# Performance work log

Measured on AMD Instinct MI355X. Metric: run time of the kernel, lower is better.

## Reference

```python
import jax, jax.numpy as jnp
import numpy as np

NUM_CLUSTERS = 10
NUM_ITERS = 10
EPS = 1e-6


def setup_inputs() -> dict:
    key = jax.random.key(0)
    k1, _ = jax.random.split(key)
    features = jax.random.normal(k1, (64, 500, 2048), dtype=jnp.float32)
    p = jnp.ones((1,), dtype=jnp.float32) * 3.0  # GeM learnable exponent
    return {"features": features, "p": p}


def reference(features, p):
    # features: [B, N, D]; k-means (10 iters) then per-cluster GeM pooling.
    B, N, D = features.shape
    K = NUM_CLUSTERS
    init_centroids = features[:, :K, :]
    f_sq = jnp.sum(features * features, axis=-1, keepdims=True)  # [B,N,1]

    def step(centroids, _):
        # squared euclidean distances [B,N,K] (argmin identical to cdist argmin)
        d2 = (f_sq
              - 2.0 * jnp.einsum('bnd,bkd->bnk', features, centroids)
              + jnp.sum(centroids * centroids, axis=-1)[:, None, :])
        assign = jnp.argmin(d2, axis=2)                      # [B,N]
        onehot = jax.nn.one_hot(assign, K, dtype=features.dtype)  # [B,N,K]
        counts = jnp.maximum(onehot.sum(axis=1), 1.0)        # [B,K]
        new_c = jnp.einsum('bnk,bnd->bkd', onehot, features) / counts[..., None]
        return new_c, assign

    centroids, assigns = jax.lax.scan(step, init_centroids, None, length=NUM_ITERS)
    # torch code uses assignments from the LAST iteration (pre-final-update centroids)
    assignments = assigns[-1]                                # [B,N]

    onehot = jax.nn.one_hot(assignments, K, dtype=features.dtype)  # [B,N,K]
    counts = onehot.sum(axis=1)                              # [B,K]
    # GeM within each cluster: mean over cluster points of clamp(x,eps)^p, then ^(1/p)
    powed = jnp.clip(features, EPS, None) ** p               # [B,N,D]
    mean_pow = jnp.einsum('bnk,bnd->bkd', onehot, powed) / jnp.maximum(counts, 1.0)[..., None]
    gem = mean_pow ** (1.0 / p)                              # [B,K,D]
    # empty clusters fall back to the centroid
    out = jnp.where((counts > 0)[..., None], gem, centroids)
    return out
```

## Files before the change

kernel.cpp:

```cpp
#include <hip/hip_runtime.h>

#define NB 64
#define NPTS 500
#define ND 2048
#define NK 10
#define NITERS 10
#define FEPS 1e-6f

__global__ __launch_bounds__(256) void init_kernel(const float* __restrict__ f,
                                                   float* __restrict__ cent,
                                                   int* __restrict__ counts)
{
    int gid = blockIdx.x * 256 + threadIdx.x;
    if (gid < NITERS * NB * NK) counts[gid] = 0;

    const int total4 = NB * NK * ND / 4;
    for (int i = gid; i < total4; i += gridDim.x * 256) {
        int d4 = i & (ND / 4 - 1);
        int bk = i >> 9;
        int b = bk / NK, k = bk - b * NK;
        ((float4*)cent)[i] =
            ((const float4*)(f + ((size_t)b * NPTS + k) * ND))[d4];
    }
}

__global__ __launch_bounds__(256) void assign_kernel(const float* __restrict__ f,
                                                     const float* __restrict__ cent,
                                                     int* __restrict__ assign,
                                                     int* __restrict__ counts_it)
{
    const int b    = blockIdx.y;
    const int wv   = threadIdx.x >> 6;
    const int lane = threadIdx.x & 63;
    const int n0   = blockIdx.x * 8 + wv * 2;
    const int n1   = n0 + 1;
    const bool v0  = (n0 < NPTS), v1 = (n1 < NPTS);

    const float4* f4 = (const float4*)(f + (size_t)b * NPTS * ND);
    const float4  z4 = make_float4(0.f, 0.f, 0.f, 0.f);
    float4 fa[8], fb[8];
#pragma unroll
    for (int j = 0; j < 8; ++j) {
        int idx = j * 64 + lane;
        fa[j] = v0 ? f4[(size_t)n0 * 512 + idx] : z4;
        fb[j] = v1 ? f4[(size_t)n1 * 512 + idx] : z4;
    }

    const float4* c4 = (const float4*)(cent + (size_t)b * NK * ND);
    float sA[NK], sB[NK];
#pragma unroll
    for (int k = 0; k < NK; ++k) {
        float a0 = 0.f, a1 = 0.f, c2 = 0.f;
#pragma unroll
        for (int j = 0; j < 8; ++j) {
            float4 c = c4[k * 512 + j * 64 + lane];
            a0 = fmaf(fa[j].x, c.x, a0); a0 = fmaf(fa[j].y, c.y, a0);
            a0 = fmaf(fa[j].z, c.z, a0); a0 = fmaf(fa[j].w, c.w, a0);
            a1 = fmaf(fb[j].x, c.x, a1); a1 = fmaf(fb[j].y, c.y, a1);
            a1 = fmaf(fb[j].z, c.z, a1); a1 = fmaf(fb[j].w, c.w, a1);
            c2 = fmaf(c.x, c.x, c2);     c2 = fmaf(c.y, c.y, c2);
            c2 = fmaf(c.z, c.z, c2);     c2 = fmaf(c.w, c.w, c2);
        }
#pragma unroll
        for (int off = 32; off > 0; off >>= 1) {
            a0 += __shfl_xor(a0, off, 64);
            a1 += __shfl_xor(a1, off, 64);
            c2 += __shfl_xor(c2, off, 64);
        }
        sA[k] = 0.5f * c2 - a0;
        sB[k] = 0.5f * c2 - a1;
    }

    int i0 = 0, i1 = 0;
    float b0 = sA[0], b1 = sB[0];
#pragma unroll
    for (int k = 1; k < NK; ++k) {
        if (sA[k] < b0) { b0 = sA[k]; i0 = k; }
        if (sB[k] < b1) { b1 = sB[k]; i1 = k; }
    }
    if (lane == 0) {
        if (v0) { assign[b * NPTS + n0] = i0; atomicAdd(&counts_it[b * NK + i0], 1); }
        if (v1) { assign[b * NPTS + n1] = i1; atomicAdd(&counts_it[b * NK + i1], 1); }
    }
}

__global__ __launch_bounds__(256) void update_kernel(const float* __restrict__ f,
                                                     const int* __restrict__ assign,
                                                     const int* __restrict__ counts_it,
                                                     float* __restrict__ cent)
{
    __shared__ int sAsn[NPTS];
    const int b = blockIdx.y;
    const int d = blockIdx.x * 256 + threadIdx.x;
    for (int i = threadIdx.x; i < NPTS; i += 256) sAsn[i] = assign[b * NPTS + i];
    __syncthreads();

    float acc[NK];
#pragma unroll
    for (int k = 0; k < NK; ++k) acc[k] = 0.f;

    const float* fp = f + (size_t)b * NPTS * ND + d;
#pragma unroll 4
    for (int n = 0; n < NPTS; ++n) {
        float v = fp[(size_t)n * ND];
        int a = sAsn[n];
#pragma unroll
        for (int k = 0; k < NK; ++k) acc[k] += (a == k) ? v : 0.f;
    }

    float* cp = cent + (size_t)b * NK * ND + d;
#pragma unroll
    for (int k = 0; k < NK; ++k) {
        float cnt = (float)counts_it[b * NK + k];
        cp[(size_t)k * ND] = acc[k] / fmaxf(cnt, 1.f);
    }
}

__global__ __launch_bounds__(256) void gem_kernel(const float* __restrict__ f,
                                                  const float* __restrict__ p_ptr,
                                                  const int* __restrict__ assign,
                                                  const int* __restrict__ counts_it,
                                                  const float* __restrict__ cent,
                                                  float* __restrict__ out)
{
    __shared__ int sAsn[NPTS];
    const int b = blockIdx.y;
    const int d = blockIdx.x * 256 + threadIdx.x;
    const float p = p_ptr[0];
    for (int i = threadIdx.x; i < NPTS; i += 256) sAsn[i] = assign[b * NPTS + i];
    __syncthreads();

    float acc[NK];
#pragma unroll
    for (int k = 0; k < NK; ++k) acc[k] = 0.f;

    const float* fp = f + (size_t)b * NPTS * ND + d;
#pragma unroll 2
    for (int n = 0; n < NPTS; ++n) {
        float v  = fp[(size_t)n * ND];
        float x  = fmaxf(v, FEPS);
        float pw = __expf(p * __logf(x));
        int a = sAsn[n];
#pragma unroll
        for (int k = 0; k < NK; ++k) acc[k] += (a == k) ? pw : 0.f;
    }

    const float invp = 1.f / p;
#pragma unroll
    for (int k = 0; k < NK; ++k) {
        int cnt = counts_it[b * NK + k];
        float res;
        if (cnt > 0) {
            float mean = acc[k] / (float)cnt;
            res = __expf(invp * __logf(mean));
        } else {
            res = cent[((size_t)b * NK + k) * ND + d];
        }
        out[((size_t)b * NK + k) * ND + d] = res;
    }
}

extern "C" void kernel_launch(void* const* d_in, const int* in_sizes, int n_in,
                              void* d_out, int out_size, void* d_ws, size_t ws_size,
                              hipStream_t stream)
{
    (void)in_sizes; (void)n_in; (void)out_size; (void)ws_size;

    const float* f = (const float*)d_in[0];
    const float* p = (const float*)d_in[1];
    float* out = (float*)d_out;

    float* cent   = (float*)d_ws;
    int*   assign = (int*)(cent + (size_t)NB * NK * ND);
    int*   counts = assign + NB * NPTS;

    init_kernel<<<160, 256, 0, stream>>>(f, cent, counts);
    for (int it = 0; it < NITERS; ++it) {
        assign_kernel<<<dim3(63, NB), 256, 0, stream>>>(f, cent, assign,
                                                        counts + it * NB * NK);
        update_kernel<<<dim3(ND / 256, NB), 256, 0, stream>>>(f, assign,
                                                              counts + it * NB * NK, cent);
    }
    gem_kernel<<<dim3(ND / 256, NB), 256, 0, stream>>>(f, p, assign,
                                                       counts + (NITERS - 1) * NB * NK,
                                                       cent, out);
}
```

Before: 2.602 ms.

## Fuse assignment and centroid accumulation into one pass with LDS atomics

After: 5.944 ms. +128.4%, slower.

```diff
diff --git a/kernel.cpp b/kernel.cpp
--- a/kernel.cpp
+++ b/kernel.cpp
@@ -6,114 +6,194 @@
 #define NK 10
 #define NITERS 10
 #define FEPS 1e-6f
+#define PPB 125
+#define ACCN (4 * NK * 512)
 
 __global__ __launch_bounds__(256) void init_kernel(const float* __restrict__ f,
                                                    float* __restrict__ cent,
-                                                   int* __restrict__ counts)
-{
-    int gid = blockIdx.x * 256 + threadIdx.x;
+                                                   float* __restrict__ cnorm,
+                                                   int* __restrict__ counts,
+                                                   float* __restrict__ sums,
+                                                   int useAtomic)
+{
+    const int bid = blockIdx.x;
+    const int b = bid / NK, k = bid - b * NK;
+    const int tid = threadIdx.x, wave = tid >> 6, lane = tid & 63;
+
+    const float4* src = (const float4*)(f + ((size_t)b * NPTS + k) * ND);
+    float4* dst = (float4*)cent + (size_t)bid * 512;
+    float4* srow = (float4*)sums + (size_t)bid * 512;
+    const float4 z4 = make_float4(0.f, 0.f, 0.f, 0.f);
+
+    float nrm = 0.f;
+    for (int i = tid; i < 512; i += 256) {
+        float4 v = src[i];
+        dst[i] = v;
+        nrm += v.x * v.x + v.y * v.y + v.z * v.z + v.w * v.w;
+        if (useAtomic) srow[i] = z4;
+    }
+#pragma unroll
+    for (int off = 32; off > 0; off >>= 1) nrm += __shfl_xor(nrm, off, 64);
+    __shared__ float red[4];
+    if (lane == 0) red[wave] = nrm;
+    __syncthreads();
+    if (tid == 0) cnorm[bid] = red[0] + red[1] + red[2] + red[3];
+
+    int gid = bid * 256 + tid;
     if (gid < NITERS * NB * NK) counts[gid] = 0;
-
-    const int total4 = NB * NK * ND / 4;
-    for (int i = gid; i < total4; i += gridDim.x * 256) {
-        int d4 = i & (ND / 4 - 1);
-        int bk = i >> 9;
-        int b = bk / NK, k = bk - b * NK;
-        ((float4*)cent)[i] =
-            ((const float4*)(f + ((size_t)b * NPTS + k) * ND))[d4];
-    }
-}
-
-__global__ __launch_bounds__(256) void assign_kernel(const float* __restrict__ f,
-                                                     const float* __restrict__ cent,
-                                                     int* __restrict__ assign,
-                                                     int* __restrict__ counts_it)
-{
-    const int b    = blockIdx.y;
-    const int wv   = threadIdx.x >> 6;
-    const int lane = threadIdx.x & 63;
-    const int n0   = blockIdx.x * 8 + wv * 2;
-    const int n1   = n0 + 1;
-    const bool v0  = (n0 < NPTS), v1 = (n1 < NPTS);
-
-    const float4* f4 = (const float4*)(f + (size_t)b * NPTS * ND);
-    const float4  z4 = make_float4(0.f, 0.f, 0.f, 0.f);
-    float4 fa[8], fb[8];
-#pragma unroll
-    for (int j = 0; j < 8; ++j) {
-        int idx = j * 64 + lane;
-        fa[j] = v0 ? f4[(size_t)n0 * 512 + idx] : z4;
-        fb[j] = v1 ? f4[(size_t)n1 * 512 + idx] : z4;
-    }
-
-    const float4* c4 = (const float4*)(cent + (size_t)b * NK * ND);
-    float sA[NK], sB[NK];
-#pragma unroll
-    for (int k = 0; k < NK; ++k) {
-        float a0 = 0.f, a1 = 0.f, c2 = 0.f;
-#pragma unroll
-        for (int j = 0; j < 8; ++j) {
-            float4 c = c4[k * 512 + j * 64 + lane];
-            a0 = fmaf(fa[j].x, c.x, a0); a0 = fmaf(fa[j].y, c.y, a0);
-            a0 = fmaf(fa[j].z, c.z, a0); a0 = fmaf(fa[j].w, c.w, a0);
-            a1 = fmaf(fb[j].x, c.x, a1); a1 = fmaf(fb[j].y, c.y, a1);
-            a1 = fmaf(fb[j].z, c.z, a1); a1 = fmaf(fb[j].w, c.w, a1);
-            c2 = fmaf(c.x, c.x, c2);     c2 = fmaf(c.y, c.y, c2);
-            c2 = fmaf(c.z, c.z, c2);     c2 = fmaf(c.w, c.w, c2);
-        }
-#pragma unroll
-        for (int off = 32; off > 0; off >>= 1) {
-            a0 += __shfl_xor(a0, off, 64);
-            a1 += __shfl_xor(a1, off, 64);
-            c2 += __shfl_xor(c2, off, 64);
-        }
-        sA[k] = 0.5f * c2 - a0;
-        sB[k] = 0.5f * c2 - a1;
-    }
-
-    int i0 = 0, i1 = 0;
-    float b0 = sA[0], b1 = sB[0];
-#pragma unroll
-    for (int k = 1; k < NK; ++k) {
-        if (sA[k] < b0) { b0 = sA[k]; i0 = k; }
-        if (sB[k] < b1) { b1 = sB[k]; i1 = k; }
-    }
-    if (lane == 0) {
-        if (v0) { assign[b * NPTS + n0] = i0; atomicAdd(&counts_it[b * NK + i0], 1); }
-        if (v1) { assign[b * NPTS + n1] = i1; atomicAdd(&counts_it[b * NK + i1], 1); }
-    }
-}
-
-__global__ __launch_bounds__(256) void update_kernel(const float* __restrict__ f,
-                                                     const int* __restrict__ assign,
-                                                     const int* __restrict__ counts_it,
-                                                     float* __restrict__ cent)
-{
-    __shared__ int sAsn[NPTS];
-    const int b = blockIdx.y;
-    const int d = blockIdx.x * 256 + threadIdx.x;
-    for (int i = threadIdx.x; i < NPTS; i += 256) sAsn[i] = assign[b * NPTS + i];
-    __syncthreads();
-
-    float acc[NK];
-#pragma unroll
-    for (int k = 0; k < NK; ++k) acc[k] = 0.f;
-
-    const float* fp = f + (size_t)b * NPTS * ND + d;
-#pragma unroll 4
-    for (int n = 0; n < NPTS; ++n) {
-        float v = fp[(size_t)n * ND];
-        int a = sAsn[n];
-#pragma unroll
-        for (int k = 0; k < NK; ++k) acc[k] += (a == k) ? v : 0.f;
-    }
-
-    float* cp = cent + (size_t)b * NK * ND + d;
-#pragma unroll
-    for (int k = 0; k < NK; ++k) {
-        float cnt = (float)counts_it[b * NK + k];
-        cp[(size_t)k * ND] = acc[k] / fmaxf(cnt, 1.f);
-    }
+}
+
+__global__ __launch_bounds__(512, 2) void fused_kernel(const float* __restrict__ f,
+                                                       const float* __restrict__ cent,
+                                                       const float* __restrict__ cnorm,
+                                                       int* __restrict__ assignG,
+                                                       int* __restrict__ counts_it,
+                                                       float* __restrict__ sums,
+                                                       float* __restrict__ partial,
+                                                       int useAtomic)
+{
+    __shared__ float accP[ACCN];
+
+    const int b = blockIdx.y, pg = blockIdx.x;
+    const int tid = threadIdx.x, wave = tid >> 6, lane = tid & 63;
+
+    for (int i = tid; i < ACCN; i += 512) accP[i] = 0.f;
+    __syncthreads();
+
+    const float4* fb4 = (const float4*)(f + (size_t)b * NPTS * ND) + (size_t)pg * PPB * 512;
+    const float4* c4  = (const float4*)(cent + (size_t)b * NK * ND);
+
+    float cn[NK];
+#pragma unroll
+    for (int k = 0; k < NK; ++k) cn[k] = cnorm[b * NK + k];
+
+    for (int s = 0; s < 4; ++s) {
+        const int p0 = s * 32 + wave * 4;
+
+        float4 R[4][8];
+#pragma unroll
+        for (int pt = 0; pt < 4; ++pt) {
+            int m = p0 + pt; if (m >= PPB) m = PPB - 1;
+            const float4* r = fb4 + (size_t)m * 512;
+#pragma unroll
+            for (int j = 0; j < 8; ++j) R[pt][j] = r[j * 64 + lane];
+        }
+
+        float d[4][NK];
+#pragma unroll
+        for (int pt = 0; pt < 4; ++pt)
+#pragma unroll
+            for (int k = 0; k < NK; ++k) d[pt][k] = 0.f;
+
+#pragma unroll
+        for (int k = 0; k < NK; ++k) {
+#pragma unroll
+            for (int j = 0; j < 8; ++j) {
+                float4 c = c4[k * 512 + j * 64 + lane];
+#pragma unroll
+                for (int pt = 0; pt < 4; ++pt) {
+                    d[pt][k] = fmaf(R[pt][j].x, c.x, d[pt][k]);
+                    d[pt][k] = fmaf(R[pt][j].y, c.y, d[pt][k]);
+                    d[pt][k] = fmaf(R[pt][j].z, c.z, d[pt][k]);
+                    d[pt][k] = fmaf(R[pt][j].w, c.w, d[pt][k]);
+                }
+            }
+        }
+
+#pragma unroll
+        for (int off = 1; off < 64; off <<= 1)
+#pragma unroll
+            for (int pt = 0; pt < 4; ++pt)
+#pragma unroll
+                for (int k = 0; k < NK; ++k)
+                    d[pt][k] += __shfl_xor(d[pt][k], off, 64);
+
+#pragma unroll
+        for (int pt = 0; pt < 4; ++pt) {
+            int a = 0;
+            float best = 0.5f * cn[0] - d[pt][0];
+#pragma unroll
+            for (int k = 1; k < NK; ++k) {
+                float t = 0.5f * cn[k] - d[pt][k];
+                if (t < best) { best = t; a = k; }
+            }
+            const bool valid = (p0 + pt < PPB);
+            if (valid) {
+                if (lane == 0) {
+                    assignG[b * NPTS + pg * PPB + p0 + pt] = a;
+                    atomicAdd(&counts_it[b * NK + a], 1);
+                }
+#pragma unroll
+                for (int j = 0; j < 8; ++j) {
+                    int q = a * 512 + j * 64 + lane;
+                    atomicAdd(&accP[0 * 5120 + q], R[pt][j].x);
+                    atomicAdd(&accP[1 * 5120 + q], R[pt][j].y);
+                    atomicAdd(&accP[2 * 5120 + q], R[pt][j].z);
+                    atomicAdd(&accP[3 * 5120 + q], R[pt][j].w);
+                }
+            }
+        }
+    }
+
+    __syncthreads();
+
+    if (useAtomic) {
+        for (int e = tid; e < ACCN; e += 512) {
+            int c = e / 5120, r = e - c * 5120;
+            int k = r >> 9, q = r & 511;
+            atomicAdd(&sums[((size_t)(b * NK + k)) * ND + q * 4 + c], accP[e]);
+        }
+    } else {
+        float4* prow = (float4*)partial + ((size_t)(b * 4 + pg)) * NK * 512;
+        for (int idx = tid; idx < NK * 512; idx += 512) {
+            float4 v = make_float4(accP[0 * 5120 + idx], accP[1 * 5120 + idx],
+                                   accP[2 * 5120 + idx], accP[3 * 5120 + idx]);
+            prow[idx] = v;
+        }
+    }
+}
+
+__global__ __launch_bounds__(256) void finalize_kernel(float* __restrict__ cent,
+                                                       float* __restrict__ cnorm,
+                                                       const int* __restrict__ counts_it,
+                                                       float* __restrict__ sums,
+                                                       const float* __restrict__ partial,
+                                                       int useAtomic)
+{
+    const int bid = blockIdx.x;
+    const int b = bid / NK, k = bid - b * NK;
+    const int tid = threadIdx.x, wave = tid >> 6, lane = tid & 63;
+
+    const float cnt = fmaxf((float)counts_it[bid], 1.f);
+    float4* crow = (float4*)cent + (size_t)bid * 512;
+    float4* srow = (float4*)sums + (size_t)bid * 512;
+    const float4* p4 = (const float4*)partial;
+    const float4 z4 = make_float4(0.f, 0.f, 0.f, 0.f);
+
+    float nrm = 0.f;
+    for (int i = tid; i < 512; i += 256) {
+        float4 s;
+        if (useAtomic) {
+            s = srow[i];
+            srow[i] = z4;
+        } else {
+            float4 p0 = p4[((size_t)(b * 4 + 0) * NK + k) * 512 + i];
+            float4 p1 = p4[((size_t)(b * 4 + 1) * NK + k) * 512 + i];
+            float4 p2 = p4[((size_t)(b * 4 + 2) * NK + k) * 512 + i];
+            float4 p3 = p4[((size_t)(b * 4 + 3) * NK + k) * 512 + i];
+            s = make_float4(p0.x + p1.x + p2.x + p3.x, p0.y + p1.y + p2.y + p3.y,
+                            p0.z + p1.z + p2.z + p3.z, p0.w + p1.w + p2.w + p3.w);
+        }
+        float4 cv = make_float4(s.x / cnt, s.y / cnt, s.z / cnt, s.w / cnt);
+        crow[i] = cv;
+        nrm += cv.x * cv.x + cv.y * cv.y + cv.z * cv.z + cv.w * cv.w;
+    }
+#pragma unroll
+    for (int off = 32; off > 0; off >>= 1) nrm += __shfl_xor(nrm, off, 64);
+    __shared__ float red[4];
+    if (lane == 0) red[wave] = nrm;
+    __syncthreads();
+    if (tid == 0) cnorm[bid] = red[0] + red[1] + red[2] + red[3];
 }
 
 __global__ __launch_bounds__(256) void gem_kernel(const float* __restrict__ f,
@@ -164,24 +244,31 @@
                               void* d_out, int out_size, void* d_ws, size_t ws_size,
                               hipStream_t stream)
 {
-    (void)in_sizes; (void)n_in; (void)out_size; (void)ws_size;
+    (void)in_sizes; (void)n_in; (void)out_size;
 
     const float* f = (const float*)d_in[0];
     const float* p = (const float*)d_in[1];
     float* out = (float*)d_out;
 
-    float* cent   = (float*)d_ws;
-    int*   assign = (int*)(cent + (size_t)NB * NK * ND);
-    int*   counts = assign + NB * NPTS;
-
-    init_kernel<<<160, 256, 0, stream>>>(f, cent, counts);
+    const size_t centN = (size_t)NB * NK * ND;
+    float* cent  = (float*)d_ws;
+    float* cnorm = cent + centN;
+    int*   counts = (int*)(cnorm + NB * NK);
+    int*   assign = counts + NITERS * NB * NK;
+    float* big    = (float*)(assign + NB * NPTS);
+    size_t baseB  = (size_t)((char*)big - (char*)d_ws);
+
+    const int useAtomic = (ws_size >= baseB + 4 * centN * sizeof(float)) ? 0 : 1;
+    float* sums    = big;
+    float* partial = big;
+
+    init_kernel<<<NB * NK, 256, 0, stream>>>(f, cent, cnorm, counts, sums, useAtomic);
     for (int it = 0; it < NITERS; ++it) {
-        assign_kernel<<<dim3(63, NB), 256, 0, stream>>>(f, cent, assign,
-                                                        counts + it * NB * NK);
-        update_kernel<<<dim3(ND / 256, NB), 256, 0, stream>>>(f, assign,
-                                                              counts + it * NB * NK, cent);
-    }
-    gem_kernel<<<dim3(ND / 256, NB), 256, 0, stream>>>(f, p, assign,
-                                                       counts + (NITERS - 1) * NB * NK,
-                                                       cent, out);
-}
+        fused_kernel<<<dim3(4, NB), 512, 0, stream>>>(
+            f, cent, cnorm, assign, counts + it * NB * NK, sums, partial, useAtomic);
+        finalize_kernel<<<NB * NK, 256, 0, stream>>>(
+            cent, cnorm, counts + it * NB * NK, sums, partial, useAtomic);
+    }
+    gem_kernel<<<dim3(ND / 256, NB), 256, 0, stream>>>(
+        f, p, assign, counts + (NITERS - 1) * NB * NK, cent, out);
+}
```
